# Kernel optimization log

Measured on AMD Instinct MI355X. Metric: run time of the kernel, lower is better.

The kernel has to match this reference:

```python
import jax, jax.numpy as jnp
import numpy as np

B, N = 256, 50000
DIMS = (3, 32, 32)


def setup_inputs() -> dict:
    key = jax.random.key(0)
    k1, k2 = jax.random.split(key)
    x = jax.random.normal(k1, (B,) + DIMS, dtype=jnp.float32)
    data = jax.random.normal(k2, (N,) + DIMS, dtype=jnp.float32)
    sigma = jnp.ones((), dtype=jnp.float32)
    return {"x": x, "sigma": sigma, "data": data}


def reference(x, sigma, data):
    # x: [B, *dims], data: [N, *dims], sigma: scalar
    x_flat = x.reshape(x.shape[0], -1)          # [B, D]
    d_flat = data.reshape(data.shape[0], -1)    # [N, D]
    # squared pairwise distances, [N, B]
    sq_diffs = (jnp.sum(x_flat * x_flat, axis=1)[None, :]
                + jnp.sum(d_flat * d_flat, axis=1)[:, None]
                - 2.0 * (d_flat @ x_flat.T))
    # softmax over the dataset axis (axis 0)
    weights = jax.nn.softmax(-sq_diffs / (2.0 * sigma ** 2), axis=0)  # [N, B]
    eps = jnp.einsum('nb,n...->b...', weights, data)                  # [B, *dims]
    return (x - eps) / sigma
```

## Files before the change

### kernel.cpp

```cpp
#include <hip/hip_runtime.h>

typedef _Float16 f16;
typedef f16 f16x8 __attribute__((ext_vector_type(8)));
typedef float f32x4 __attribute__((ext_vector_type(4)));

static constexpr int NDATA = 50000;
static constexpr int DF    = 3072;
static constexpr int BP    = 256;
static constexpr int NW    = 50688;
static constexpr int NGRPQ = 396;
static constexpr int NDT2  = 48;

static constexpr size_t OFF_W  = 0;
static constexpr size_t OFF_XH = 25952256;
static constexpr size_t OFF_MP = 27525120;
static constexpr size_t OFF_LP = 27930624;
static constexpr size_t OFF_M  = 28336128;
static constexpr size_t OFF_L  = 28337152;
static constexpr size_t OFF_P  = 28338176;
static constexpr size_t SLAB   = (size_t)BP * DF * 4;

__device__ __forceinline__ void barrier_lgkm() {
  __builtin_amdgcn_sched_barrier(0);
  asm volatile("s_waitcnt lgkmcnt(0)" ::: "memory");
  __builtin_amdgcn_s_barrier();
  __builtin_amdgcn_sched_barrier(0);
}

__global__ void k_prep_x(const float* __restrict__ x, f16* __restrict__ xh) {
  int i = blockIdx.x * 256 + threadIdx.x;
  f32x4 v = ((const f32x4*)x)[i];
  f16 h0 = (f16)v[0], h1 = (f16)v[1], h2 = (f16)v[2], h3 = (f16)v[3];
  f16x8 dummy;
  short4* o = (short4*)xh;
  union { f16 f[4]; short4 s; } u;
  u.f[0] = h0; u.f[1] = h1; u.f[2] = h2; u.f[3] = h3;
  o[i] = u.s;
  (void)dummy;
}

__global__ __launch_bounds__(512, 4) void k_qk(const float* __restrict__ data,
                                               const f16* __restrict__ xh,
                                               const float* __restrict__ sigma,
                                               f16* __restrict__ W,
                                               float* __restrict__ Mp,
                                               float* __restrict__ Lp) {
  __shared__ char smem[61952];
  f16 (*As)[5120]  = (f16(*)[5120])smem;
  f16 (*Bs)[10240] = (f16(*)[10240])(smem + 20480);
  float* dn_s = (float*)(smem + 61440);
  float* m4   = (float*)smem;
  float* l4   = (float*)(smem + 4096);
  float* m_s  = (float*)(smem + 8192);
  f16*  trans = (f16*)(smem + 20480);

  const int tid = threadIdx.x;
  const int wid = tid >> 6, lane = tid & 63;
  const int l15 = lane & 15, kg = lane >> 4;
  const int wr = wid >> 1, wb = wid & 1;
  const int n0 = blockIdx.x * 128;

  const int arow = tid >> 2, ak = (tid & 3) * 8;
  const int ar_g = n0 + arow;
  const float* ap = data + (size_t)(ar_g < NDATA ? ar_g : NDATA - 1) * DF + ak;
  const int brow = tid >> 1, bk = (tid & 1) * 16;
  const f16* bp = xh + (size_t)brow * DF + bk;

  f32x4 acc[2][8] = {};
  float sq = 0.f;
  f32x4 a0A, a1A, a0B, a1B;
  f16x8 rb0, rb1;

  auto gloadA = [&](int k0, f32x4& a0, f32x4& a1) {
    a0 = *(const f32x4*)(ap + k0);
    a1 = *(const f32x4*)(ap + k0 + 4);
  };
  auto gloadB = [&](int k0) {
    rb0 = *(const f16x8*)(bp + k0);
    rb1 = *(const f16x8*)(bp + k0 + 8);
  };
  auto swriteA = [&](int buf, f32x4& a0, f32x4& a1) {
    f16x8 h;
#pragma unroll
    for (int j = 0; j < 4; ++j) {
      h[j] = (f16)a0[j];     sq = fmaf(a0[j], a0[j], sq);
      h[4 + j] = (f16)a1[j]; sq = fmaf(a1[j], a1[j], sq);
    }
    *(f16x8*)(&As[buf][arow * 40 + ak]) = h;
  };
  auto swriteB = [&](int buf) {
    *(f16x8*)(&Bs[buf][brow * 40 + bk]) = rb0;
    *(f16x8*)(&Bs[buf][brow * 40 + bk + 8]) = rb1;
  };
  auto compute = [&](int buf) {
    f16x8 af0 = *(const f16x8*)(&As[buf][(wr * 32 + l15) * 40 + kg * 8]);
    f16x8 af1 = *(const f16x8*)(&As[buf][(wr * 32 + 16 + l15) * 40 + kg * 8]);
#pragma unroll
    for (int c = 0; c < 8; ++c) {
      f16x8 bf = *(const f16x8*)(&Bs[buf][(wb * 128 + c * 16 + l15) * 40 + kg * 8]);
      acc[0][c] = __builtin_amdgcn_mfma_f32_16x16x32_f16(af0, bf, acc[0][c], 0, 0, 0);
      acc[1][c] = __builtin_amdgcn_mfma_f32_16x16x32_f16(af1, bf, acc[1][c], 0, 0, 0);
    }
  };

  gloadA(0, a0A, a1A);
  gloadB(0);
  swriteA(0, a0A, a1A);
  swriteB(0);
  gloadA(32, a0B, a1B);
  barrier_lgkm();

  for (int ks = 0; ks < 96; ks += 2) {
    if (ks + 2 < 96) gloadA((ks + 2) * 32, a0A, a1A);
    gloadB((ks + 1) * 32);
    compute(0);
    swriteA(1, a0B, a1B);
    swriteB(1);
    barrier_lgkm();
    if (ks + 3 < 96) { gloadA((ks + 3) * 32, a0B, a1B); }
    if (ks + 2 < 96) { gloadB((ks + 2) * 32); }
    compute(1);
    if (ks + 2 < 96) { swriteA(0, a0A, a1A); swriteB(0); }
    barrier_lgkm();
  }

  sq += __shfl_xor(sq, 1);
  sq += __shfl_xor(sq, 2);
  if ((lane & 3) == 0) dn_s[arow] = sq;
  __syncthreads();

  const float sg  = sigma[0];
  const float inv = 0.5f / (sg * sg);
  float dn[2][4];
  bool ok[2][4];
#pragma unroll
  for (int i = 0; i < 2; ++i)
#pragma unroll
    for (int r = 0; r < 4; ++r) {
      int rl = wr * 32 + i * 16 + kg * 4 + r;
      dn[i][r] = dn_s[rl];
      ok[i][r] = (n0 + rl) < NDATA;
    }

  float pm[8];
#pragma unroll
  for (int c = 0; c < 8; ++c) pm[c] = -1e30f;
#pragma unroll
  for (int i = 0; i < 2; ++i)
#pragma unroll
    for (int r = 0; r < 4; ++r)
#pragma unroll
      for (int c = 0; c < 8; ++c) {
        float v = ok[i][r] ? (2.f * acc[i][c][r] - dn[i][r]) * inv : -1e30f;
        pm[c] = fmaxf(pm[c], v);
      }
#pragma unroll
  for (int c = 0; c < 8; ++c) {
    pm[c] = fmaxf(pm[c], __shfl_xor(pm[c], 16));
    pm[c] = fmaxf(pm[c], __shfl_xor(pm[c], 32));
  }
  if (kg == 0) {
#pragma unroll
    for (int c = 0; c < 8; ++c) m4[wr * 256 + wb * 128 + c * 16 + l15] = pm[c];
  }
  __syncthreads();
  if (tid < 256)
    m_s[tid] = fmaxf(fmaxf(m4[tid], m4[256 + tid]), fmaxf(m4[512 + tid], m4[768 + tid]));
  __syncthreads();

  float mcol[8];
#pragma unroll
  for (int c = 0; c < 8; ++c) mcol[c] = m_s[wb * 128 + c * 16 + l15];

  float pl[8] = {};
#pragma unroll
  for (int h = 0; h < 2; ++h) {
    if ((wr >> 1) == h) {
#pragma unroll
      for (int i = 0; i < 2; ++i)
#pragma unroll
        for (int r = 0; r < 4; ++r) {
          const int rl2 = (wr & 1) * 32 + i * 16 + kg * 4 + r;
#pragma unroll
          for (int c = 0; c < 8; ++c) {
            float v = (2.f * acc[i][c][r] - dn[i][r]) * inv;
            float w = ok[i][r] ? __expf(v - mcol[c]) : 0.f;
            pl[c] += w;
            trans[(wb * 128 + c * 16 + l15) * 72 + rl2] = (f16)w;
          }
        }
    }
    __syncthreads();
    {
      const int col = tid >> 1, q = tid & 1;
      const f16* src = trans + col * 72 + q * 32;
      f16* dst = W + (size_t)col * NW + n0 + h * 64 + q * 32;
#pragma unroll
      for (int j = 0; j < 4; ++j)
        *(f16x8*)(dst + j * 8) = *(const f16x8*)(src + j * 8);
    }
    __syncthreads();
  }

#pragma unroll
  for (int c = 0; c < 8; ++c) {
    pl[c] += __shfl_xor(pl[c], 16);
    pl[c] += __shfl_xor(pl[c], 32);
  }
  if (kg == 0) {
#pragma unroll
    for (int c = 0; c < 8; ++c) l4[wr * 256 + wb * 128 + c * 16 + l15] = pl[c];
  }
  __syncthreads();
  if (tid < 256) {
    Mp[blockIdx.x * 256 + tid] = m_s[tid];
    Lp[blockIdx.x * 256 + tid] = l4[tid] + l4[256 + tid] + l4[512 + tid] + l4[768 + tid];
  }
}

__global__ void k_comb(const float* __restrict__ Mp, const float* __restrict__ Lp,
                       float* __restrict__ M, float* __restrict__ L, int ngrp) {
  __shared__ float ms[4][256], ls[4][256];
  const int tid = threadIdx.x;
  const int q = tid >> 8, b = tid & 255;
  float m = -1e38f, l = 0.f;
  for (int g = q; g < ngrp; g += 4) {
    float m2 = Mp[g * 256 + b], l2 = Lp[g * 256 + b];
    if (m2 > m) { l = l * __expf(m - m2) + l2; m = m2; }
    else        { l += l2 * __expf(m2 - m); }
  }
  ms[q][b] = m; ls[q][b] = l;
  __syncthreads();
  if (q == 0) {
#pragma unroll
    for (int j = 1; j < 4; ++j) {
      float m2 = ms[j][b], l2 = ls[j][b];
      if (m2 > m) { l = l * __expf(m - m2) + l2; m = m2; }
      else        { l += l2 * __expf(m2 - m); }
    }
    M[b] = m; L[b] = l;
  }
}

__global__ __launch_bounds__(512, 4) void k_pv(const float* __restrict__ data,
                                               const f16* __restrict__ W,
                                               const float* __restrict__ Mp,
                                               const float* __restrict__ M,
                                               float* __restrict__ part,
                                               int chn, int per8) {
  __shared__ f16 T[2][64 * 40];
  const int tid = threadIdx.x;
  const int wid = tid >> 6, lane = tid & 63;
  const int l15 = lane & 15, kg = lane >> 4;
  const int bid = blockIdx.x;
  const int swz = (bid & 7) * per8 + (bid >> 3);
  const int chunk = swz / NDT2;
  const int dt = swz % NDT2;
  const int d0 = dt * 64;
  const int nstart = chunk * chn;
  const int kst = chn >> 5;
  const int nl = tid >> 4, dl = (tid & 15) * 4;

  f32x4 acc[2][4] = {};
  const int b0 = wid * 32 + l15, b1 = b0 + 16;
  const float Mb0 = M[b0], Mb1 = M[b1];
  const f16* wp0 = W + (size_t)b0 * NW + nstart + kg * 8;
  const f16* wp1 = W + (size_t)b1 * NW + nstart + kg * 8;

  f32x4 gA, gB;
  f16x8 w0c, w1c, w0n, w1n;
  float mpAc, mpBc, mpAn, mpBn;

  auto gload = [&](int ks, f32x4& g) {
    int row = nstart + ks * 32 + nl;
    int rc = row < NDATA ? row : NDATA - 1;
    g = *(const f32x4*)(data + (size_t)rc * DF + d0 + dl);
  };
  auto wload = [&](int ks, f16x8& w0, f16x8& w1, float& ma, float& mb) {
    w0 = *(const f16x8*)(wp0 + ks * 32);
    w1 = *(const f16x8*)(wp1 + ks * 32);
    int gq = (nstart + ks * 32) >> 7;
    ma = Mp[gq * 256 + b0];
    mb = Mp[gq * 256 + b1];
  };
  auto twrite = [&](int buf, f32x4& g) {
#pragma unroll
    for (int j = 0; j < 4; ++j) {
      int d = dl + j;
      int pn = nl ^ (((d >> 3) & 3) << 3);
      T[buf][d * 40 + pn] = (f16)g[j];
    }
  };
  auto compute = [&](int buf, f16x8& w0, f16x8& w1, float ma, float mb) {
    f16 h0 = (f16)__expf(ma - Mb0);
    f16 h1 = (f16)__expf(mb - Mb1);
    f16x8 a0, a1;
#pragma unroll
    for (int j = 0; j < 8; ++j) { a0[j] = w0[j] * h0; a1[j] = w1[j] * h1; }
#pragma unroll
    for (int c = 0; c < 4; ++c) {
      int d = c * 16 + l15;
      int pb = (kg * 8) ^ (((d >> 3) & 3) << 3);
      f16x8 bf = *(const f16x8*)(&T[buf][d * 40 + pb]);
      acc[0][c] = __builtin_amdgcn_mfma_f32_16x16x32_f16(a0, bf, acc[0][c], 0, 0, 0);
      acc[1][c] = __builtin_amdgcn_mfma_f32_16x16x32_f16(a1, bf, acc[1][c], 0, 0, 0);
    }
  };

  gload(0, gA);
  wload(0, w0c, w1c, mpAc, mpBc);
  twrite(0, gA);
  gload(1, gB);
  barrier_lgkm();

  for (int ks = 0; ks < kst; ks += 2) {
    if (ks + 2 < kst) gload(ks + 2, gA);
    if (ks + 1 < kst) wload(ks + 1, w0n, w1n, mpAn, mpBn);
    compute(0, w0c, w1c, mpAc, mpBc);
    if (ks + 1 < kst) twrite(1, gB);
    barrier_lgkm();
    if (ks + 1 < kst) {
      if (ks + 3 < kst) gload(ks + 3, gB);
      if (ks + 2 < kst) wload(ks + 2, w0c, w1c, mpAc, mpBc);
      compute(1, w0n, w1n, mpAn, mpBn);
      if (ks + 2 < kst) twrite(0, gA);
      barrier_lgkm();
    }
  }

  float* pp = part + (size_t)chunk * (BP * DF);
#pragma unroll
  for (int i = 0; i < 2; ++i)
#pragma unroll
    for (int c = 0; c < 4; ++c)
#pragma unroll
      for (int r = 0; r < 4; ++r) {
        int b = wid * 32 + i * 16 + kg * 4 + r;
        int d = d0 + c * 16 + l15;
        pp[(size_t)b * DF + d] = acc[i][c][r];
      }
}

__global__ void k_final(const float* __restrict__ x, const float* __restrict__ sigma,
                        const float* __restrict__ part, const float* __restrict__ L,
                        float* __restrict__ out, int nch) {
  int i = blockIdx.x * 256 + threadIdx.x;
  int b = (i * 4) / DF;
  f32x4 s = {};
  for (int c = 0; c < nch; ++c) s += ((const f32x4*)(part + (size_t)c * BP * DF))[i];
  f32x4 xv = ((const f32x4*)x)[i];
  float invL = 1.f / L[b];
  float invsg = 1.f / sigma[0];
  f32x4 r;
#pragma unroll
  for (int j = 0; j < 4; ++j) r[j] = (xv[j] - s[j] * invL) * invsg;
  ((f32x4*)out)[i] = r;
}

extern "C" void kernel_launch(void* const* d_in, const int* in_sizes, int n_in,
                              void* d_out, int out_size, void* d_ws, size_t ws_size,
                              hipStream_t stream) {
  const float* x     = (const float*)d_in[0];
  const float* sigma = (const float*)d_in[1];
  const float* data  = (const float*)d_in[2];
  float* out = (float*)d_out;
  char* ws = (char*)d_ws;

  f16*   W  = (f16*)(ws + OFF_W);
  f16*   xh = (f16*)(ws + OFF_XH);
  float* Mp = (float*)(ws + OFF_MP);
  float* Lp = (float*)(ws + OFF_LP);
  float* M  = (float*)(ws + OFF_M);
  float* L  = (float*)(ws + OFF_L);
  float* P  = (float*)(ws + OFF_P);

  int nch = 24, chn = 2112;
  if (ws_size < OFF_P + 24 * SLAB) { nch = 16; chn = 3168; }
  if (ws_size < OFF_P + 16 * SLAB) { nch = 8;  chn = 6336; }
  const int grid_pv = NDT2 * nch;
  const int per8 = grid_pv / 8;

  k_prep_x<<<768, 256, 0, stream>>>(x, xh);
  k_qk<<<NGRPQ, 512, 0, stream>>>(data, xh, sigma, W, Mp, Lp);
  k_comb<<<1, 1024, 0, stream>>>(Mp, Lp, M, L, NGRPQ);
  k_pv<<<grid_pv, 512, 0, stream>>>(data, W, Mp, M, P, chn, per8);
  k_final<<<768, 256, 0, stream>>>(x, sigma, P, L, out, nch);
}
```

Measured before the change: 522.3 us.

## Stream QK tiles via direct global-to-LDS loads and pack PV transposes

The QK kernel now fills shared memory through global_load_lds DMA, with XOR-swizzled fp32 A tiles and f16 B tiles, instead of staging loads through registers. The fp16 conversion and squared-norm accumulation move into the compute step, and synchronisation is driven by vmcnt waits across a two-deep prefetch. The PV kernel's transposed data writes pack two rows into one 32-bit LDS store instead of four scalar f16 stores. The aim is to cut VGPR staging and LDS store instruction count. The cost is more LDS space for fp32 A tiles, per-step conversion work in the MFMA loop, and two barriers per k-step.

```diff
diff --git a/kernel.cpp b/kernel.cpp
--- a/kernel.cpp
+++ b/kernel.cpp
@@ -3,6 +3,7 @@
 typedef _Float16 f16;
 typedef f16 f16x8 __attribute__((ext_vector_type(8)));
 typedef float f32x4 __attribute__((ext_vector_type(4)));
+typedef float f32x2 __attribute__((ext_vector_type(2)));
 
 static constexpr int NDATA = 50000;
 static constexpr int DF    = 3072;
@@ -20,6 +21,13 @@
 static constexpr size_t OFF_P  = 28338176;
 static constexpr size_t SLAB   = (size_t)BP * DF * 4;
 
+__device__ __forceinline__ void dma16(const void* g, void* l) {
+  __builtin_amdgcn_global_load_lds(
+      (const __attribute__((address_space(1))) void*)(uintptr_t)g,
+      (__attribute__((address_space(3))) void*)(uint32_t)(uintptr_t)l,
+      16, 0, 0);
+}
+
 __device__ __forceinline__ void barrier_lgkm() {
   __builtin_amdgcn_sched_barrier(0);
   asm volatile("s_waitcnt lgkmcnt(0)" ::: "memory");
@@ -30,13 +38,9 @@
 __global__ void k_prep_x(const float* __restrict__ x, f16* __restrict__ xh) {
   int i = blockIdx.x * 256 + threadIdx.x;
   f32x4 v = ((const f32x4*)x)[i];
-  f16 h0 = (f16)v[0], h1 = (f16)v[1], h2 = (f16)v[2], h3 = (f16)v[3];
-  f16x8 dummy;
-  short4* o = (short4*)xh;
   union { f16 f[4]; short4 s; } u;
-  u.f[0] = h0; u.f[1] = h1; u.f[2] = h2; u.f[3] = h3;
-  o[i] = u.s;
-  (void)dummy;
+  u.f[0] = (f16)v[0]; u.f[1] = (f16)v[1]; u.f[2] = (f16)v[2]; u.f[3] = (f16)v[3];
+  ((short4*)xh)[i] = u.s;
 }
 
 __global__ __launch_bounds__(512, 4) void k_qk(const float* __restrict__ data,
@@ -45,10 +49,10 @@
                                                f16* __restrict__ W,
                                                float* __restrict__ Mp,
                                                float* __restrict__ Lp) {
-  __shared__ char smem[61952];
-  f16 (*As)[5120]  = (f16(*)[5120])smem;
-  f16 (*Bs)[10240] = (f16(*)[10240])(smem + 20480);
-  float* dn_s = (float*)(smem + 61440);
+  __shared__ char smem[66048];
+  float* Asm = (float*)smem;
+  f16*   Bsm = (f16*)(smem + 32768);
+  float* dn_s = (float*)(smem + 65536);
   float* m4   = (float*)smem;
   float* l4   = (float*)(smem + 4096);
   float* m_s  = (float*)(smem + 8192);
@@ -60,73 +64,83 @@
   const int wr = wid >> 1, wb = wid & 1;
   const int n0 = blockIdx.x * 128;
 
-  const int arow = tid >> 2, ak = (tid & 3) * 8;
-  const int ar_g = n0 + arow;
-  const float* ap = data + (size_t)(ar_g < NDATA ? ar_g : NDATA - 1) * DF + ak;
-  const int brow = tid >> 1, bk = (tid & 1) * 16;
-  const f16* bp = xh + (size_t)brow * DF + bk;
+  const int rA0 = wid * 16 + (lane >> 3);
+  const int rA1 = rA0 + 8;
+  const int gA0 = (n0 + rA0) < NDATA ? (n0 + rA0) : NDATA - 1;
+  const int gA1 = (n0 + rA1) < NDATA ? (n0 + rA1) : NDATA - 1;
+  const float* pA0 = data + (size_t)gA0 * DF + ((lane & 7) ^ (rA0 & 7)) * 4;
+  const float* pA1 = data + (size_t)gA1 * DF + ((lane & 7) ^ (rA1 & 7)) * 4;
+  const int rB0 = wid * 32 + (lane >> 2);
+  const int rB1 = rB0 + 16;
+  const f16* pB0 = xh + (size_t)rB0 * DF + ((lane & 3) ^ ((rB0 >> 1) & 3)) * 8;
+  const f16* pB1 = xh + (size_t)rB1 * DF + ((lane & 3) ^ ((rB1 >> 1) & 3)) * 8;
+  float* lA0 = Asm + (size_t)(wid * 16) * 32;
+  float* lA1 = Asm + (size_t)(wid * 16 + 8) * 32;
+  f16*   lB0 = Bsm + (size_t)(wid * 32) * 32;
+  f16*   lB1 = Bsm + (size_t)(wid * 32 + 16) * 32;
+
+  auto issue = [&](int buf, int k0) {
+    dma16(pA0 + k0, lA0 + buf * 4096);
+    dma16(pA1 + k0, lA1 + buf * 4096);
+    dma16(pB0 + k0, lB0 + buf * 8192);
+    dma16(pB1 + k0, lB1 + buf * 8192);
+  };
 
   f32x4 acc[2][8] = {};
-  float sq = 0.f;
-  f32x4 a0A, a1A, a0B, a1B;
-  f16x8 rb0, rb1;
-
-  auto gloadA = [&](int k0, f32x4& a0, f32x4& a1) {
-    a0 = *(const f32x4*)(ap + k0);
-    a1 = *(const f32x4*)(ap + k0 + 4);
-  };
-  auto gloadB = [&](int k0) {
-    rb0 = *(const f16x8*)(bp + k0);
-    rb1 = *(const f16x8*)(bp + k0 + 8);
-  };
-  auto swriteA = [&](int buf, f32x4& a0, f32x4& a1) {
-    f16x8 h;
+  float sq0 = 0.f, sq1 = 0.f;
+  const int r0 = wr * 32 + l15, r1 = r0 + 16;
+  const int sA = l15 & 7;
+  const int pc0 = (kg * 2) ^ sA, pc1 = (kg * 2 + 1) ^ sA;
+
+  auto compute = [&](int buf) {
+    const float* Ab = Asm + buf * 4096;
+    const f16*   Bb = Bsm + buf * 8192;
+    f32x4 a00 = *(const f32x4*)(Ab + r0 * 32 + pc0 * 4);
+    f32x4 a01 = *(const f32x4*)(Ab + r0 * 32 + pc1 * 4);
+    f32x4 a10 = *(const f32x4*)(Ab + r1 * 32 + pc0 * 4);
+    f32x4 a11 = *(const f32x4*)(Ab + r1 * 32 + pc1 * 4);
+    f16x8 af0, af1;
 #pragma unroll
     for (int j = 0; j < 4; ++j) {
-      h[j] = (f16)a0[j];     sq = fmaf(a0[j], a0[j], sq);
-      h[4 + j] = (f16)a1[j]; sq = fmaf(a1[j], a1[j], sq);
-    }
-    *(f16x8*)(&As[buf][arow * 40 + ak]) = h;
-  };
-  auto swriteB = [&](int buf) {
-    *(f16x8*)(&Bs[buf][brow * 40 + bk]) = rb0;
-    *(f16x8*)(&Bs[buf][brow * 40 + bk + 8]) = rb1;
-  };
-  auto compute = [&](int buf) {
-    f16x8 af0 = *(const f16x8*)(&As[buf][(wr * 32 + l15) * 40 + kg * 8]);
-    f16x8 af1 = *(const f16x8*)(&As[buf][(wr * 32 + 16 + l15) * 40 + kg * 8]);
+      af0[j] = (f16)a00[j]; af0[4 + j] = (f16)a01[j];
+      af1[j] = (f16)a10[j]; af1[4 + j] = (f16)a11[j];
+    }
+    if (wb == 0) {
+#pragma unroll
+      for (int j = 0; j < 4; ++j) {
+        sq0 = fmaf(a00[j], a00[j], sq0); sq0 = fmaf(a01[j], a01[j], sq0);
+        sq1 = fmaf(a10[j], a10[j], sq1); sq1 = fmaf(a11[j], a11[j], sq1);
+      }
+    }
 #pragma unroll
     for (int c = 0; c < 8; ++c) {
-      f16x8 bf = *(const f16x8*)(&Bs[buf][(wb * 128 + c * 16 + l15) * 40 + kg * 8]);
+      const int b = wb * 128 + c * 16 + l15;
+      f16x8 bf = *(const f16x8*)(Bb + b * 32 + ((kg ^ ((b >> 1) & 3)) * 8));
       acc[0][c] = __builtin_amdgcn_mfma_f32_16x16x32_f16(af0, bf, acc[0][c], 0, 0, 0);
       acc[1][c] = __builtin_amdgcn_mfma_f32_16x16x32_f16(af1, bf, acc[1][c], 0, 0, 0);
     }
   };
 
-  gloadA(0, a0A, a1A);
-  gloadB(0);
-  swriteA(0, a0A, a1A);
-  swriteB(0);
-  gloadA(32, a0B, a1B);
-  barrier_lgkm();
-
-  for (int ks = 0; ks < 96; ks += 2) {
-    if (ks + 2 < 96) gloadA((ks + 2) * 32, a0A, a1A);
-    gloadB((ks + 1) * 32);
-    compute(0);
-    swriteA(1, a0B, a1B);
-    swriteB(1);
-    barrier_lgkm();
-    if (ks + 3 < 96) { gloadA((ks + 3) * 32, a0B, a1B); }
-    if (ks + 2 < 96) { gloadB((ks + 2) * 32); }
-    compute(1);
-    if (ks + 2 < 96) { swriteA(0, a0A, a1A); swriteB(0); }
-    barrier_lgkm();
-  }
-
-  sq += __shfl_xor(sq, 1);
-  sq += __shfl_xor(sq, 2);
-  if ((lane & 3) == 0) dn_s[arow] = sq;
+  issue(0, 0);
+  issue(1, 32);
+
+  for (int k = 0; k < 96; ++k) {
+    __builtin_amdgcn_sched_barrier(0);
+    if (k < 95) asm volatile("s_waitcnt vmcnt(4)" ::: "memory");
+    else        asm volatile("s_waitcnt vmcnt(0)" ::: "memory");
+    __builtin_amdgcn_s_barrier();
+    __builtin_amdgcn_sched_barrier(0);
+    compute(k & 1);
+    __builtin_amdgcn_sched_barrier(0);
+    asm volatile("s_waitcnt lgkmcnt(0)" ::: "memory");
+    __builtin_amdgcn_s_barrier();
+    __builtin_amdgcn_sched_barrier(0);
+    if (k + 2 < 96) issue(k & 1, (k + 2) * 32);
+  }
+
+  sq0 += __shfl_xor(sq0, 16); sq0 += __shfl_xor(sq0, 32);
+  sq1 += __shfl_xor(sq1, 16); sq1 += __shfl_xor(sq1, 32);
+  if (wb == 0 && kg == 0) { dn_s[r0] = sq0; dn_s[r1] = sq1; }
   __syncthreads();
 
   const float sg  = sigma[0];
@@ -259,7 +273,8 @@
   const int d0 = dt * 64;
   const int nstart = chunk * chn;
   const int kst = chn >> 5;
-  const int nl = tid >> 4, dl = (tid & 15) * 4;
+  const int np = tid >> 5;
+  const int d2 = (tid & 31) * 2;
 
   f32x4 acc[2][4] = {};
   const int b0 = wid * 32 + l15, b1 = b0 + 16;
@@ -267,14 +282,16 @@
   const f16* wp0 = W + (size_t)b0 * NW + nstart + kg * 8;
   const f16* wp1 = W + (size_t)b1 * NW + nstart + kg * 8;
 
-  f32x4 gA, gB;
+  f32x2 gaA, gbA, gaB, gbB;
   f16x8 w0c, w1c, w0n, w1n;
   float mpAc, mpBc, mpAn, mpBn;
 
-  auto gload = [&](int ks, f32x4& g) {
-    int row = nstart + ks * 32 + nl;
-    int rc = row < NDATA ? row : NDATA - 1;
-    g = *(const f32x4*)(data + (size_t)rc * DF + d0 + dl);
+  auto gload = [&](int ks, f32x2& ga, f32x2& gb) {
+    int n = nstart + ks * 32 + np * 2;
+    int na = n < NDATA ? n : NDATA - 1;
+    int nb = (n + 1) < NDATA ? (n + 1) : NDATA - 1;
+    ga = *(const f32x2*)(data + (size_t)na * DF + d0 + d2);
+    gb = *(const f32x2*)(data + (size_t)nb * DF + d0 + d2);
   };
   auto wload = [&](int ks, f16x8& w0, f16x8& w1, float& ma, float& mb) {
     w0 = *(const f16x8*)(wp0 + ks * 32);
@@ -283,13 +300,14 @@
     ma = Mp[gq * 256 + b0];
     mb = Mp[gq * 256 + b1];
   };
-  auto twrite = [&](int buf, f32x4& g) {
-#pragma unroll
-    for (int j = 0; j < 4; ++j) {
-      int d = dl + j;
-      int pn = nl ^ (((d >> 3) & 3) << 3);
-      T[buf][d * 40 + pn] = (f16)g[j];
-    }
+  auto twrite = [&](int buf, f32x2& ga, f32x2& gb) {
+    uint32_t* Tw = (uint32_t*)&T[buf][0];
+    int pn = np ^ (((d2 >> 3) & 3) << 2);
+    union { f16 f[2]; uint32_t u; } u0, u1;
+    u0.f[0] = (f16)ga[0]; u0.f[1] = (f16)gb[0];
+    u1.f[0] = (f16)ga[1]; u1.f[1] = (f16)gb[1];
+    Tw[d2 * 20 + pn] = u0.u;
+    Tw[(d2 + 1) * 20 + pn] = u1.u;
   };
   auto compute = [&](int buf, f16x8& w0, f16x8& w1, float ma, float mb) {
     f16 h0 = (f16)__expf(ma - Mb0);
@@ -307,23 +325,23 @@
     }
   };
 
-  gload(0, gA);
+  gload(0, gaA, gbA);
   wload(0, w0c, w1c, mpAc, mpBc);
-  twrite(0, gA);
-  gload(1, gB);
+  twrite(0, gaA, gbA);
+  gload(1, gaB, gbB);
   barrier_lgkm();
 
   for (int ks = 0; ks < kst; ks += 2) {
-    if (ks + 2 < kst) gload(ks + 2, gA);
+    if (ks + 2 < kst) gload(ks + 2, gaA, gbA);
     if (ks + 1 < kst) wload(ks + 1, w0n, w1n, mpAn, mpBn);
     compute(0, w0c, w1c, mpAc, mpBc);
-    if (ks + 1 < kst) twrite(1, gB);
+    if (ks + 1 < kst) twrite(1, gaB, gbB);
     barrier_lgkm();
     if (ks + 1 < kst) {
-      if (ks + 3 < kst) gload(ks + 3, gB);
+      if (ks + 3 < kst) gload(ks + 3, gaB, gbB);
       if (ks + 2 < kst) wload(ks + 2, w0c, w1c, mpAc, mpBc);
       compute(1, w0n, w1n, mpAn, mpBn);
-      if (ks + 2 < kst) twrite(0, gA);
+      if (ks + 2 < kst) twrite(0, gaA, gbA);
       barrier_lgkm();
     }
   }
```

Result: slower. 543.5 us (+4.0%).

## Split QK and PV kernels into smaller 256-thread blocks over batch halves

Applied to the files above, without the earlier changes.

The QK kernel now uses 256-thread blocks that each handle 64 data rows and half of the batch columns, with a swizzled block index, so four times as many smaller blocks are launched. The PV kernel is likewise split across two batch halves with 256 threads, and packs pairs of data rows into 32-bit LDS words. Partial max and sum buffers are re-laid out for 64-row groups. The goal is better occupancy and load balance across CUs, at the cost of re-reading the data matrix twice in QK and more blocks overall.

```diff
diff --git a/kernel.cpp b/kernel.cpp
--- a/kernel.cpp
+++ b/kernel.cpp
@@ -7,17 +7,16 @@
 static constexpr int NDATA = 50000;
 static constexpr int DF    = 3072;
 static constexpr int BP    = 256;
+static constexpr int NGRPQ = 792;
 static constexpr int NW    = 50688;
-static constexpr int NGRPQ = 396;
-static constexpr int NDT2  = 48;
 
 static constexpr size_t OFF_W  = 0;
 static constexpr size_t OFF_XH = 25952256;
 static constexpr size_t OFF_MP = 27525120;
-static constexpr size_t OFF_LP = 27930624;
-static constexpr size_t OFF_M  = 28336128;
-static constexpr size_t OFF_L  = 28337152;
-static constexpr size_t OFF_P  = 28338176;
+static constexpr size_t OFF_LP = 28336128;
+static constexpr size_t OFF_M  = 29147136;
+static constexpr size_t OFF_L  = 29148160;
+static constexpr size_t OFF_P  = 29149184;
 static constexpr size_t SLAB   = (size_t)BP * DF * 4;
 
 __device__ __forceinline__ void barrier_lgkm() {
@@ -30,56 +29,55 @@
 __global__ void k_prep_x(const float* __restrict__ x, f16* __restrict__ xh) {
   int i = blockIdx.x * 256 + threadIdx.x;
   f32x4 v = ((const f32x4*)x)[i];
-  f16 h0 = (f16)v[0], h1 = (f16)v[1], h2 = (f16)v[2], h3 = (f16)v[3];
-  f16x8 dummy;
-  short4* o = (short4*)xh;
   union { f16 f[4]; short4 s; } u;
-  u.f[0] = h0; u.f[1] = h1; u.f[2] = h2; u.f[3] = h3;
-  o[i] = u.s;
-  (void)dummy;
-}
-
-__global__ __launch_bounds__(512, 4) void k_qk(const float* __restrict__ data,
-                                               const f16* __restrict__ xh,
-                                               const float* __restrict__ sigma,
-                                               f16* __restrict__ W,
-                                               float* __restrict__ Mp,
-                                               float* __restrict__ Lp) {
-  __shared__ char smem[61952];
-  f16 (*As)[5120]  = (f16(*)[5120])smem;
-  f16 (*Bs)[10240] = (f16(*)[10240])(smem + 20480);
-  float* dn_s = (float*)(smem + 61440);
+  u.f[0] = (f16)v[0]; u.f[1] = (f16)v[1]; u.f[2] = (f16)v[2]; u.f[3] = (f16)v[3];
+  ((short4*)xh)[i] = u.s;
+}
+
+__global__ __launch_bounds__(256) void k_qk(const float* __restrict__ data,
+                                            const f16* __restrict__ xh,
+                                            const float* __restrict__ sigma,
+                                            f16* __restrict__ W,
+                                            float* __restrict__ Mp,
+                                            float* __restrict__ Lp) {
+  __shared__ char smem[31232];
+  f16 (*As)[2560] = (f16(*)[2560])smem;
+  f16 (*Bs)[5120] = (f16(*)[5120])(smem + 10240);
+  float* dn_s = (float*)(smem + 30720);
   float* m4   = (float*)smem;
-  float* l4   = (float*)(smem + 4096);
-  float* m_s  = (float*)(smem + 8192);
-  f16*  trans = (f16*)(smem + 20480);
+  float* l4   = (float*)(smem + 2048);
+  float* m_s  = (float*)(smem + 4096);
+  f16*  trans = (f16*)(smem + 10240);
 
   const int tid = threadIdx.x;
   const int wid = tid >> 6, lane = tid & 63;
   const int l15 = lane & 15, kg = lane >> 4;
-  const int wr = wid >> 1, wb = wid & 1;
-  const int n0 = blockIdx.x * 128;
+  const int bid = blockIdx.x;
+  const int swz = (bid & 7) * 198 + (bid >> 3);
+  const int g   = swz >> 1;
+  const int bh  = swz & 1;
+  const int n0  = g * 64;
 
   const int arow = tid >> 2, ak = (tid & 3) * 8;
-  const int ar_g = n0 + arow;
-  const float* ap = data + (size_t)(ar_g < NDATA ? ar_g : NDATA - 1) * DF + ak;
+  const int agr = n0 + arow;
+  const float* ap = data + (size_t)(agr < NDATA ? agr : NDATA - 1) * DF + ak;
   const int brow = tid >> 1, bk = (tid & 1) * 16;
-  const f16* bp = xh + (size_t)brow * DF + bk;
-
-  f32x4 acc[2][8] = {};
+  const f16* bp = xh + (size_t)(bh * 128 + brow) * DF + bk;
+
+  f32x4 acc[8] = {};
   float sq = 0.f;
-  f32x4 a0A, a1A, a0B, a1B;
-  f16x8 rb0, rb1;
+  f32x4 aA0, aA1, aB0, aB1;
+  f16x8 bA0, bA1, bB0, bB1;
 
   auto gloadA = [&](int k0, f32x4& a0, f32x4& a1) {
     a0 = *(const f32x4*)(ap + k0);
     a1 = *(const f32x4*)(ap + k0 + 4);
   };
-  auto gloadB = [&](int k0) {
-    rb0 = *(const f16x8*)(bp + k0);
-    rb1 = *(const f16x8*)(bp + k0 + 8);
-  };
-  auto swriteA = [&](int buf, f32x4& a0, f32x4& a1) {
+  auto gloadB = [&](int k0, f16x8& b0, f16x8& b1) {
+    b0 = *(const f16x8*)(bp + k0);
+    b1 = *(const f16x8*)(bp + k0 + 8);
+  };
+  auto swrite = [&](int buf, f32x4& a0, f32x4& a1, f16x8& b0, f16x8& b1) {
     f16x8 h;
 #pragma unroll
     for (int j = 0; j < 4; ++j) {
@@ -87,73 +85,60 @@
       h[4 + j] = (f16)a1[j]; sq = fmaf(a1[j], a1[j], sq);
     }
     *(f16x8*)(&As[buf][arow * 40 + ak]) = h;
-  };
-  auto swriteB = [&](int buf) {
-    *(f16x8*)(&Bs[buf][brow * 40 + bk]) = rb0;
-    *(f16x8*)(&Bs[buf][brow * 40 + bk + 8]) = rb1;
+    *(f16x8*)(&Bs[buf][brow * 40 + bk]) = b0;
+    *(f16x8*)(&Bs[buf][brow * 40 + bk + 8]) = b1;
   };
   auto compute = [&](int buf) {
-    f16x8 af0 = *(const f16x8*)(&As[buf][(wr * 32 + l15) * 40 + kg * 8]);
-    f16x8 af1 = *(const f16x8*)(&As[buf][(wr * 32 + 16 + l15) * 40 + kg * 8]);
+    f16x8 af = *(const f16x8*)(&As[buf][(wid * 16 + l15) * 40 + kg * 8]);
 #pragma unroll
     for (int c = 0; c < 8; ++c) {
-      f16x8 bf = *(const f16x8*)(&Bs[buf][(wb * 128 + c * 16 + l15) * 40 + kg * 8]);
-      acc[0][c] = __builtin_amdgcn_mfma_f32_16x16x32_f16(af0, bf, acc[0][c], 0, 0, 0);
-      acc[1][c] = __builtin_amdgcn_mfma_f32_16x16x32_f16(af1, bf, acc[1][c], 0, 0, 0);
-    }
-  };
-
-  gloadA(0, a0A, a1A);
-  gloadB(0);
-  swriteA(0, a0A, a1A);
-  swriteB(0);
-  gloadA(32, a0B, a1B);
+      f16x8 bf = *(const f16x8*)(&Bs[buf][(c * 16 + l15) * 40 + kg * 8]);
+      acc[c] = __builtin_amdgcn_mfma_f32_16x16x32_f16(af, bf, acc[c], 0, 0, 0);
+    }
+  };
+
+  gloadA(0, aA0, aA1); gloadB(0, bA0, bA1);
+  swrite(0, aA0, aA1, bA0, bA1);
+  gloadA(32, aB0, aB1); gloadB(32, bB0, bB1);
   barrier_lgkm();
 
   for (int ks = 0; ks < 96; ks += 2) {
-    if (ks + 2 < 96) gloadA((ks + 2) * 32, a0A, a1A);
-    gloadB((ks + 1) * 32);
+    if (ks + 2 < 96) { gloadA((ks + 2) * 32, aA0, aA1); gloadB((ks + 2) * 32, bA0, bA1); }
     compute(0);
-    swriteA(1, a0B, a1B);
-    swriteB(1);
+    swrite(1, aB0, aB1, bB0, bB1);
     barrier_lgkm();
-    if (ks + 3 < 96) { gloadA((ks + 3) * 32, a0B, a1B); }
-    if (ks + 2 < 96) { gloadB((ks + 2) * 32); }
+    if (ks + 3 < 96) { gloadA((ks + 3) * 32, aB0, aB1); gloadB((ks + 3) * 32, bB0, bB1); }
     compute(1);
-    if (ks + 2 < 96) { swriteA(0, a0A, a1A); swriteB(0); }
+    if (ks + 2 < 96) swrite(0, aA0, aA1, bA0, bA1);
     barrier_lgkm();
   }
 
   sq += __shfl_xor(sq, 1);
   sq += __shfl_xor(sq, 2);
-  if ((lane & 3) == 0) dn_s[arow] = sq;
+  if ((tid & 3) == 0) dn_s[arow] = sq;
   __syncthreads();
 
   const float sg  = sigma[0];
   const float inv = 0.5f / (sg * sg);
-  float dn[2][4];
-  bool ok[2][4];
-#pragma unroll
-  for (int i = 0; i < 2; ++i)
-#pragma unroll
-    for (int r = 0; r < 4; ++r) {
-      int rl = wr * 32 + i * 16 + kg * 4 + r;
-      dn[i][r] = dn_s[rl];
-      ok[i][r] = (n0 + rl) < NDATA;
-    }
+  float dn[4];
+  bool ok[4];
+#pragma unroll
+  for (int r = 0; r < 4; ++r) {
+    const int rl = wid * 16 + kg * 4 + r;
+    dn[r] = dn_s[rl];
+    ok[r] = (n0 + rl) < NDATA;
+  }
 
   float pm[8];
 #pragma unroll
   for (int c = 0; c < 8; ++c) pm[c] = -1e30f;
 #pragma unroll
-  for (int i = 0; i < 2; ++i)
-#pragma unroll
-    for (int r = 0; r < 4; ++r)
-#pragma unroll
-      for (int c = 0; c < 8; ++c) {
-        float v = ok[i][r] ? (2.f * acc[i][c][r] - dn[i][r]) * inv : -1e30f;
-        pm[c] = fmaxf(pm[c], v);
-      }
+  for (int r = 0; r < 4; ++r)
+#pragma unroll
+    for (int c = 0; c < 8; ++c) {
+      float v = ok[r] ? (2.f * acc[c][r] - dn[r]) * inv : -1e30f;
+      pm[c] = fmaxf(pm[c], v);
+    }
 #pragma unroll
   for (int c = 0; c < 8; ++c) {
     pm[c] = fmaxf(pm[c], __shfl_xor(pm[c], 16));
@@ -161,47 +146,29 @@
   }
   if (kg == 0) {
 #pragma unroll
-    for (int c = 0; c < 8; ++c) m4[wr * 256 + wb * 128 + c * 16 + l15] = pm[c];
-  }
-  __syncthreads();
-  if (tid < 256)
-    m_s[tid] = fmaxf(fmaxf(m4[tid], m4[256 + tid]), fmaxf(m4[512 + tid], m4[768 + tid]));
+    for (int c = 0; c < 8; ++c) m4[wid * 128 + c * 16 + l15] = pm[c];
+  }
+  __syncthreads();
+  if (tid < 128)
+    m_s[tid] = fmaxf(fmaxf(m4[tid], m4[128 + tid]), fmaxf(m4[256 + tid], m4[384 + tid]));
   __syncthreads();
 
   float mcol[8];
 #pragma unroll
-  for (int c = 0; c < 8; ++c) mcol[c] = m_s[wb * 128 + c * 16 + l15];
+  for (int c = 0; c < 8; ++c) mcol[c] = m_s[c * 16 + l15];
 
   float pl[8] = {};
 #pragma unroll
-  for (int h = 0; h < 2; ++h) {
-    if ((wr >> 1) == h) {
-#pragma unroll
-      for (int i = 0; i < 2; ++i)
-#pragma unroll
-        for (int r = 0; r < 4; ++r) {
-          const int rl2 = (wr & 1) * 32 + i * 16 + kg * 4 + r;
-#pragma unroll
-          for (int c = 0; c < 8; ++c) {
-            float v = (2.f * acc[i][c][r] - dn[i][r]) * inv;
-            float w = ok[i][r] ? __expf(v - mcol[c]) : 0.f;
-            pl[c] += w;
-            trans[(wb * 128 + c * 16 + l15) * 72 + rl2] = (f16)w;
-          }
-        }
-    }
-    __syncthreads();
-    {
-      const int col = tid >> 1, q = tid & 1;
-      const f16* src = trans + col * 72 + q * 32;
-      f16* dst = W + (size_t)col * NW + n0 + h * 64 + q * 32;
-#pragma unroll
-      for (int j = 0; j < 4; ++j)
-        *(f16x8*)(dst + j * 8) = *(const f16x8*)(src + j * 8);
-    }
-    __syncthreads();
-  }
-
+  for (int r = 0; r < 4; ++r) {
+    const int rl = wid * 16 + kg * 4 + r;
+#pragma unroll
+    for (int c = 0; c < 8; ++c) {
+      float v = (2.f * acc[c][r] - dn[r]) * inv;
+      float w = ok[r] ? __expf(v - mcol[c]) : 0.f;
+      pl[c] += w;
+      trans[(c * 16 + l15) * 72 + rl] = (f16)w;
+    }
+  }
 #pragma unroll
   for (int c = 0; c < 8; ++c) {
     pl[c] += __shfl_xor(pl[c], 16);
@@ -209,12 +176,20 @@
   }
   if (kg == 0) {
 #pragma unroll
-    for (int c = 0; c < 8; ++c) l4[wr * 256 + wb * 128 + c * 16 + l15] = pl[c];
-  }
-  __syncthreads();
-  if (tid < 256) {
-    Mp[blockIdx.x * 256 + tid] = m_s[tid];
-    Lp[blockIdx.x * 256 + tid] = l4[tid] + l4[256 + tid] + l4[512 + tid] + l4[768 + tid];
+    for (int c = 0; c < 8; ++c) l4[wid * 128 + c * 16 + l15] = pl[c];
+  }
+  __syncthreads();
+  if (tid < 128) {
+    Mp[g * 256 + bh * 128 + tid] = m_s[tid];
+    Lp[g * 256 + bh * 128 + tid] = l4[tid] + l4[128 + tid] + l4[256 + tid] + l4[384 + tid];
+  }
+  {
+    const int col = tid >> 1, q = tid & 1;
+    const f16* src = trans + col * 72 + q * 32;
+    f16* dst = W + (size_t)(bh * 128 + col) * NW + n0 + q * 32;
+#pragma unroll
+    for (int j = 0; j < 4; ++j)
+      *(f16x8*)(dst + j * 8) = *(const f16x8*)(src + j * 8);
   }
 }
 
@@ -242,53 +217,59 @@
   }
 }
 
-__global__ __launch_bounds__(512, 4) void k_pv(const float* __restrict__ data,
-                                               const f16* __restrict__ W,
-                                               const float* __restrict__ Mp,
-                                               const float* __restrict__ M,
-                                               float* __restrict__ part,
-                                               int chn, int per8) {
-  __shared__ f16 T[2][64 * 40];
+__global__ __launch_bounds__(256) void k_pv(const float* __restrict__ data,
+                                            const f16* __restrict__ W,
+                                            const float* __restrict__ Mp,
+                                            const float* __restrict__ M,
+                                            float* __restrict__ part,
+                                            int chn, int per8) {
+  __shared__ uint32_t T[2][64 * 20];
   const int tid = threadIdx.x;
   const int wid = tid >> 6, lane = tid & 63;
   const int l15 = lane & 15, kg = lane >> 4;
   const int bid = blockIdx.x;
   const int swz = (bid & 7) * per8 + (bid >> 3);
-  const int chunk = swz / NDT2;
-  const int dt = swz % NDT2;
+  const int chunk = swz / 96;
+  const int r96 = swz % 96;
+  const int dt = r96 >> 1, bh = r96 & 1;
   const int d0 = dt * 64;
   const int nstart = chunk * chn;
   const int kst = chn >> 5;
-  const int nl = tid >> 4, dl = (tid & 15) * 4;
+  const int np = tid >> 4;
+  const int d4 = (tid & 15) * 4;
 
   f32x4 acc[2][4] = {};
-  const int b0 = wid * 32 + l15, b1 = b0 + 16;
+  const int b0 = bh * 128 + wid * 32 + l15, b1 = b0 + 16;
   const float Mb0 = M[b0], Mb1 = M[b1];
   const f16* wp0 = W + (size_t)b0 * NW + nstart + kg * 8;
   const f16* wp1 = W + (size_t)b1 * NW + nstart + kg * 8;
 
-  f32x4 gA, gB;
+  f32x4 gaA, gbA, gaB, gbB;
   f16x8 w0c, w1c, w0n, w1n;
   float mpAc, mpBc, mpAn, mpBn;
 
-  auto gload = [&](int ks, f32x4& g) {
-    int row = nstart + ks * 32 + nl;
-    int rc = row < NDATA ? row : NDATA - 1;
-    g = *(const f32x4*)(data + (size_t)rc * DF + d0 + dl);
+  auto gload = [&](int ks, f32x4& ga, f32x4& gb) {
+    int n = nstart + ks * 32 + np * 2;
+    int na = n < NDATA ? n : NDATA - 1;
+    int nb = (n + 1) < NDATA ? (n + 1) : NDATA - 1;
+    ga = *(const f32x4*)(data + (size_t)na * DF + d0 + d4);
+    gb = *(const f32x4*)(data + (size_t)nb * DF + d0 + d4);
   };
   auto wload = [&](int ks, f16x8& w0, f16x8& w1, float& ma, float& mb) {
     w0 = *(const f16x8*)(wp0 + ks * 32);
     w1 = *(const f16x8*)(wp1 + ks * 32);
-    int gq = (nstart + ks * 32) >> 7;
+    int gq = (nstart + ks * 32) >> 6;
     ma = Mp[gq * 256 + b0];
     mb = Mp[gq * 256 + b1];
   };
-  auto twrite = [&](int buf, f32x4& g) {
+  auto twrite = [&](int buf, f32x4& ga, f32x4& gb) {
 #pragma unroll
     for (int j = 0; j < 4; ++j) {
-      int d = dl + j;
-      int pn = nl ^ (((d >> 3) & 3) << 3);
-      T[buf][d * 40 + pn] = (f16)g[j];
+      int d = d4 + j;
+      int pn = np ^ (((d >> 3) & 3) << 2);
+      union { f16 f[2]; uint32_t u; } u;
+      u.f[0] = (f16)ga[j]; u.f[1] = (f16)gb[j];
+      T[buf][d * 20 + pn] = u.u;
     }
   };
   auto compute = [&](int buf, f16x8& w0, f16x8& w1, float ma, float mb) {
@@ -300,30 +281,30 @@
 #pragma unroll
     for (int c = 0; c < 4; ++c) {
       int d = c * 16 + l15;
-      int pb = (kg * 8) ^ (((d >> 3) & 3) << 3);
-      f16x8 bf = *(const f16x8*)(&T[buf][d * 40 + pb]);
+      int dw = d * 20 + ((kg * 4) ^ (((d >> 3) & 3) << 2));
+      f16x8 bf = *(const f16x8*)(&T[buf][dw]);
       acc[0][c] = __builtin_amdgcn_mfma_f32_16x16x32_f16(a0, bf, acc[0][c], 0, 0, 0);
       acc[1][c] = __builtin_amdgcn_mfma_f32_16x16x32_f16(a1, bf, acc[1][c], 0, 0, 0);
     }
   };
 
-  gload(0, gA);
+  gload(0, gaA, gbA);
   wload(0, w0c, w1c, mpAc, mpBc);
-  twrite(0, gA);
-  gload(1, gB);
+  twrite(0, gaA, gbA);
+  gload(1, gaB, gbB);
   barrier_lgkm();
 
   for (int ks = 0; ks < kst; ks += 2) {
-    if (ks + 2 < kst) gload(ks + 2, gA);
+    if (ks + 2 < kst) gload(ks + 2, gaA, gbA);
     if (ks + 1 < kst) wload(ks + 1, w0n, w1n, mpAn, mpBn);
     compute(0, w0c, w1c, mpAc, mpBc);
-    if (ks + 1 < kst) twrite(1, gB);
+    if (ks + 1 < kst) twrite(1, gaB, gbB);
     barrier_lgkm();
     if (ks + 1 < kst) {
-      if (ks + 3 < kst) gload(ks + 3, gB);
+      if (ks + 3 < kst) gload(ks + 3, gaB, gbB);
       if (ks + 2 < kst) wload(ks + 2, w0c, w1c, mpAc, mpBc);
       compute(1, w0n, w1n, mpAn, mpBn);
-      if (ks + 2 < kst) twrite(0, gA);
+      if (ks + 2 < kst) twrite(0, gaA, gbA);
       barrier_lgkm();
     }
   }
@@ -335,7 +316,7 @@
     for (int c = 0; c < 4; ++c)
 #pragma unroll
       for (int r = 0; r < 4; ++r) {
-        int b = wid * 32 + i * 16 + kg * 4 + r;
+        int b = bh * 128 + wid * 32 + i * 16 + kg * 4 + r;
         int d = d0 + c * 16 + l15;
         pp[(size_t)b * DF + d] = acc[i][c][r];
       }
@@ -377,12 +358,12 @@
   int nch = 24, chn = 2112;
   if (ws_size < OFF_P + 24 * SLAB) { nch = 16; chn = 3168; }
   if (ws_size < OFF_P + 16 * SLAB) { nch = 8;  chn = 6336; }
-  const int grid_pv = NDT2 * nch;
+  const int grid_pv = 96 * nch;
   const int per8 = grid_pv / 8;
 
   k_prep_x<<<768, 256, 0, stream>>>(x, xh);
-  k_qk<<<NGRPQ, 512, 0, stream>>>(data, xh, sigma, W, Mp, Lp);
+  k_qk<<<NGRPQ * 2, 256, 0, stream>>>(data, xh, sigma, W, Mp, Lp);
   k_comb<<<1, 1024, 0, stream>>>(Mp, Lp, M, L, NGRPQ);
-  k_pv<<<grid_pv, 512, 0, stream>>>(data, W, Mp, M, P, chn, per8);
+  k_pv<<<grid_pv, 256, 0, stream>>>(data, W, Mp, M, P, chn, per8);
   k_final<<<768, 256, 0, stream>>>(x, sigma, P, L, out, nch);
 }
```

Measured after the change: 674.5 us. 1.29x slower.
